# Kernel tuning notes

Hardware: AMD Instinct MI355X
Metric: run time of the kernel (lower is better)

## Reference

```python
import jax, jax.numpy as jnp
from jax import lax
import numpy as np

B, S, G = 16, 384, 384
N = S + G
E_CHAR, D = 100, 128
H = D // 2              # LSTM hidden per direction
NHEAD, NHID = 4, 64
T = 21                  # crf_input_dim = label_alphabet.size() + 1
START, STOP = T - 2, T - 1
ALPHA = 0.2
CHAR_V, GAZ_V = 8000, 100000
NEG = -9e15             # pyGAT masked_fill value


def setup_inputs():
    key = jax.random.key(0)
    ks = jax.random.split(key, 20)
    f32 = jnp.float32
    def nrm(k, shape, s=0.05):
        return (jax.random.normal(k, shape) * s).astype(f32)
    eye = jnp.eye(N, dtype=bool)
    def adj(k):
        return ((jax.random.uniform(k, (B, N, N)) < 0.1) | eye[None]).astype(jnp.int32)
    return dict(
        batch_char=jax.random.randint(ks[0], (B, S), 0, CHAR_V),
        batch_len=jnp.full((B,), S, jnp.int32),
        gaz_list=jax.random.randint(ks[1], (B, G), 0, GAZ_V),
        t_graph=adj(ks[2]), c_graph=adj(ks[3]), l_graph=adj(ks[4]),
        mask=jnp.ones((B, S), jnp.int32),
        char_table=nrm(ks[5], (CHAR_V, E_CHAR)),
        gaz_table=nrm(ks[6], (GAZ_V, D)),
        w_ih_f=nrm(ks[7], (4 * H, E_CHAR)), w_hh_f=nrm(ks[8], (4 * H, H)),
        b_f=jnp.zeros((4 * H,), f32),
        w_ih_b=nrm(ks[9], (4 * H, E_CHAR)), w_hh_b=nrm(ks[10], (4 * H, H)),
        b_b=jnp.zeros((4 * H,), f32),
        h2h_W=nrm(ks[11], (T, D)), h2h_b=jnp.zeros((T,), f32),
        gat_Wh=nrm(ks[12], (3, NHEAD, D, NHID)),
        gat_ah=nrm(ks[13], (3, NHEAD, 2 * NHID)),
        gat_Wo=nrm(ks[14], (3, NHEAD * NHID, T)),
        gat_ao=nrm(ks[15], (3, 2 * T)),
        fuse_w=jnp.ones((4,), f32),
        transitions=nrm(ks[16], (T, T)),
    )


def _lstm_dir(x, w_ih, w_hh, b, reverse):
    # x: [B,S,E]; torch gate order i,f,g,o
    Bb = x.shape[0]
    Hh = w_hh.shape[1]
    xw = jnp.einsum('bse,ge->bsg', x, w_ih) + b
    def step(carry, xt):
        h, c = carry
        g = xt + h @ w_hh.T
        i, f, gg, o = jnp.split(g, 4, axis=-1)
        c = jax.nn.sigmoid(f) * c + jax.nn.sigmoid(i) * jnp.tanh(gg)
        h = jax.nn.sigmoid(o) * jnp.tanh(c)
        return (h, c), h
    h0 = jnp.zeros((Bb, Hh), x.dtype)
    _, hs = lax.scan(step, (h0, h0), xw.swapaxes(0, 1), reverse=reverse)
    return hs.swapaxes(0, 1)


def _gat_layer(x, adj, W, a, concat):
    # pyGAT batched layer: e_ij = LeakyReLU(a . [Wh_i || Wh_j]), masked softmax over j
    h = jnp.einsum('bnd,df->bnf', x, W)
    F_ = W.shape[1]
    f1 = h @ a[:F_]           # [B,N]
    f2 = h @ a[F_:]
    e = jax.nn.leaky_relu(f1[:, :, None] + f2[:, None, :], negative_slope=ALPHA)
    e = jnp.where(adj > 0, e, NEG)
    att = jax.nn.softmax(e, axis=-1)
    out = jnp.einsum('bij,bjf->bif', att, h)
    return jax.nn.elu(out) if concat else out


def _gat(x, adj, Wh, ah, Wo, ao):
    heads = jax.vmap(lambda W, a: _gat_layer(x, adj, W, a, True))(Wh, ah)  # [H,B,N,F]
    hcat = jnp.moveaxis(heads, 0, 2).reshape(x.shape[0], x.shape[1], -1)
    return jax.nn.elu(_gat_layer(hcat, adj, Wo, ao, False))


def _crf_feature(batch_char, gaz_list, graphs, char_table, gaz_table,
                 w_ih_f, w_hh_f, b_f, w_ih_b, w_hh_b, b_b, h2h_W, h2h_b,
                 gat_Wh, gat_ah, gat_Wo, gat_ao, fuse_w):
    emb = char_table[batch_char]                      # [B,S,E_CHAR]
    hf = _lstm_dir(emb, w_ih_f, w_hh_f, b_f, False)
    hb = _lstm_dir(emb, w_ih_b, w_hh_b, b_b, True)
    lstm_feat = jnp.concatenate([hf, hb], axis=-1)    # [B,S,D]
    gaz_feat = gaz_table[gaz_list]                    # [B,G,D]
    gat_in = jnp.concatenate([lstm_feat, gaz_feat], axis=1)  # [B,N,D]
    gat_outs = [_gat(gat_in, adj, gat_Wh[k], gat_ah[k], gat_Wo[k], gat_ao[k])[:, :S]
                for k, adj in enumerate(graphs)]
    lstm_proj = lstm_feat @ h2h_W.T + h2h_b           # [B,S,T]
    return (fuse_w[0] * lstm_proj + fuse_w[1] * gat_outs[0]
            + fuse_w[2] * gat_outs[1] + fuse_w[3] * gat_outs[2])


def _viterbi(feats, transitions, mask):
    Bb, Ss, Tt = feats.shape
    ids = jnp.arange(Tt)
    part0 = feats[:, 0, :] + transitions[START][None, :]
    def step(part, inp):
        feat_t, m_t = inp
        cur = part[:, :, None] + transitions[None] + feat_t[:, None, :]  # [B,prev,cur]
        new = cur.max(axis=1)
        bp = cur.argmax(axis=1)
        m = (m_t > 0)[:, None]
        return jnp.where(m, new, part), jnp.where(m, bp, ids[None, :])
    part, bps = lax.scan(step, part0,
                         (feats[:, 1:].swapaxes(0, 1), mask[:, 1:].swapaxes(0, 1)))
    last_tag = jnp.argmax(part + transitions[:, STOP][None, :], axis=1)
    def back(tag, bp):
        prev = jnp.take_along_axis(bp, tag[:, None], axis=1)[:, 0]
        return prev, prev
    _, prevs = lax.scan(back, last_tag, bps, reverse=True)   # prevs[j] = tag at time j
    return jnp.concatenate([prevs.swapaxes(0, 1), last_tag[:, None]], axis=1)


def reference(batch_char, batch_len, gaz_list, t_graph, c_graph, l_graph, mask,
              char_table, gaz_table, w_ih_f, w_hh_f, b_f, w_ih_b, w_hh_b, b_b,
              h2h_W, h2h_b, gat_Wh, gat_ah, gat_Wo, gat_ao, fuse_w, transitions):
    # batch_len is all == S (mask all ones), so packed BiLSTM == plain BiLSTM
    feats = _crf_feature(batch_char, gaz_list, (t_graph, c_graph, l_graph),
                         char_table, gaz_table, w_ih_f, w_hh_f, b_f,
                         w_ih_b, w_hh_b, b_b, h2h_W, h2h_b,
                         gat_Wh, gat_ah, gat_Wo, gat_ao, fuse_w)
    return _viterbi(feats, transitions, mask)
```

## Files before the change

kernel.cpp:

```cpp
#include <hip/hip_runtime.h>
#include <hip/hip_bf16.h>
#include <cstdint>
#include <cstddef>

#define BB 16
#define SS 384
#define GG 384
#define NN 768
#define DD 128
#define EC 100
#define TT 21
#define NHEADS 4
#define BN (BB*NN)
#define BS (BB*SS)

typedef float v2f __attribute__((ext_vector_type(2)));

__device__ __forceinline__ float sigf(float x) { return 1.0f / (1.0f + __expf(-x)); }
__device__ __forceinline__ float tanh_fast(float x) {
    return 1.0f - 2.0f / (__expf(2.0f * x) + 1.0f);
}
__device__ __forceinline__ float wred_max(float v) {
    #pragma unroll
    for (int o = 32; o > 0; o >>= 1) v = fmaxf(v, __shfl_xor(v, o));
    return v;
}
__device__ __forceinline__ float wred_sum(float v) {
    #pragma unroll
    for (int o = 32; o > 0; o >>= 1) v += __shfl_xor(v, o);
    return v;
}
__device__ __forceinline__ float rlane(float v, int l) {
    return __uint_as_float(__builtin_amdgcn_readlane(__float_as_uint(v), l));
}

__global__ __launch_bounds__(256) void k_xw(
    const int* __restrict__ batch_char, const float* __restrict__ char_table,
    const float* __restrict__ w_ih_f, const float* __restrict__ b_f,
    const float* __restrict__ w_ih_b, const float* __restrict__ b_b,
    float* __restrict__ xw_f, float* __restrict__ xw_b)
{
    __shared__ float At[EC * 68];
    __shared__ float Bt[EC * 68];
    __shared__ int   chs[64];
    const int tid = threadIdx.x;
    const int rt  = blockIdx.x;
    const int ot  = blockIdx.y;
    const int dir = ot >> 2, gt = ot & 3;
    const float* wih  = dir ? w_ih_b : w_ih_f;
    const float* bias = dir ? b_b    : b_f;
    float*       out  = dir ? xw_b   : xw_f;

    if (tid < 64) chs[tid] = batch_char[rt * 64 + tid];
    __syncthreads();
    for (int idx = tid; idx < 64 * EC; idx += 256) {
        int r = idx / EC, e = idx - r * EC;
        At[e * 68 + r] = char_table[(size_t)chs[r] * EC + e];
        Bt[e * 68 + r] = wih[(size_t)(gt * 64 + r) * EC + e];
    }
    __syncthreads();

    const int ty = tid >> 4, tx = tid & 15;
    const int r0 = ty * 4, c0 = tx * 4;
    float acc[4][4] = {};
    #pragma unroll 4
    for (int e = 0; e < EC; ++e) {
        float4 a = *(const float4*)&At[e * 68 + r0];
        float4 bv = *(const float4*)&Bt[e * 68 + c0];
        float av[4] = {a.x, a.y, a.z, a.w};
        float bb[4] = {bv.x, bv.y, bv.z, bv.w};
        #pragma unroll
        for (int i = 0; i < 4; ++i)
            #pragma unroll
            for (int j = 0; j < 4; ++j) acc[i][j] = fmaf(av[i], bb[j], acc[i][j]);
    }
    #pragma unroll
    for (int i = 0; i < 4; ++i) {
        int row = rt * 64 + r0 + i;
        int gc  = gt * 64 + c0;
        float4 o;
        o.x = acc[i][0] + bias[gc + 0];
        o.y = acc[i][1] + bias[gc + 1];
        o.z = acc[i][2] + bias[gc + 2];
        o.w = acc[i][3] + bias[gc + 3];
        *(float4*)&out[(size_t)row * 256 + gc] = o;
    }
}

__global__ __launch_bounds__(256) void k_gaz(
    const int* __restrict__ gaz_list, const float* __restrict__ gaz_table,
    float* __restrict__ gat_in)
{
    int idx = blockIdx.x * 256 + threadIdx.x;
    int d = idx & 127;
    int rest = idx >> 7;
    int g = rest % GG;
    int b = rest / GG;
    float v = gaz_table[(size_t)gaz_list[b * GG + g] * DD + d];
    gat_in[((size_t)b * NN + SS + g) * DD + d] = v;
}

__global__ __launch_bounds__(64, 1) void k_lstm(
    const float* __restrict__ xw_f, const float* __restrict__ xw_b,
    const float* __restrict__ w_hh_f, const float* __restrict__ w_hh_b,
    float* __restrict__ gat_in)
{
    const int lane = threadIdx.x;
    const int b = blockIdx.x >> 1, dir = blockIdx.x & 1;
    const float* xw  = (dir ? xw_b : xw_f) + (size_t)b * SS * 256;
    const float* whh = dir ? w_hh_b : w_hh_f;

    v2f w2[4][32];
    #pragma unroll
    for (int g = 0; g < 4; ++g) {
        const float4* r4 = (const float4*)(whh + (size_t)(g * 64 + lane) * 64);
        #pragma unroll
        for (int q = 0; q < 16; ++q) {
            float4 v = r4[q];
            w2[g][2 * q]     = v2f{v.x, v.y};
            w2[g][2 * q + 1] = v2f{v.z, v.w};
        }
    }

    float h = 0.f, c = 0.f;
    const int t0 = dir ? (SS - 1) : 0;
    float x0 = xw[t0 * 256 +   0 + lane];
    float x1 = xw[t0 * 256 +  64 + lane];
    float x2 = xw[t0 * 256 + 128 + lane];
    float x3 = xw[t0 * 256 + 192 + lane];
    float* outp = gat_in + ((size_t)b * NN) * DD + dir * 64 + lane;

    for (int tt = 0; tt < SS; ++tt) {
        const int t = dir ? (SS - 1 - tt) : tt;
        const int tn = dir ? (t - 1) : (t + 1);
        float nx0 = 0.f, nx1 = 0.f, nx2 = 0.f, nx3 = 0.f;
        if (tt + 1 < SS) {
            nx0 = xw[tn * 256 +   0 + lane];
            nx1 = xw[tn * 256 +  64 + lane];
            nx2 = xw[tn * 256 + 128 + lane];
            nx3 = xw[tn * 256 + 192 + lane];
        }
        v2f a0 = v2f{x0, 0.f}, a1 = v2f{x1, 0.f};
        v2f a2 = v2f{x2, 0.f}, a3 = v2f{x3, 0.f};
        #pragma unroll
        for (int j = 0; j < 32; ++j) {
            v2f hp = v2f{rlane(h, 2 * j), rlane(h, 2 * j + 1)};
            a0 = __builtin_elementwise_fma(hp, w2[0][j], a0);
            a1 = __builtin_elementwise_fma(hp, w2[1][j], a1);
            a2 = __builtin_elementwise_fma(hp, w2[2][j], a2);
            a3 = __builtin_elementwise_fma(hp, w2[3][j], a3);
        }
        float gi = a0.x + a0.y, gf = a1.x + a1.y;
        float gg = a2.x + a2.y, go = a3.x + a3.y;
        float nc = sigf(gf) * c + sigf(gi) * tanh_fast(gg);
        h = sigf(go) * tanh_fast(nc);
        c = nc;
        outp[(size_t)t * DD] = h;
        x0 = nx0; x1 = nx1; x2 = nx2; x3 = nx3;
    }
}

__global__ __launch_bounds__(256) void k_p1(
    const float* __restrict__ gat_in, const float* __restrict__ gat_Wh,
    const float* __restrict__ gat_ah, int k,
    float* __restrict__ h1, float* __restrict__ f1g, float* __restrict__ f2g)
{
    __shared__ float At[64 * 68];
    __shared__ float Bt[64 * 68];
    __shared__ float sf1[64], sf2[64];
    const int tid = threadIdx.x;
    const int rt = blockIdx.x, hd = blockIdx.y;
    if (tid < 64) { sf1[tid] = 0.f; sf2[tid] = 0.f; }
    const float* W = gat_Wh + ((size_t)(k * NHEADS + hd)) * DD * 64;
    const int ty = tid >> 4, tx = tid & 15;
    const int r0 = ty * 4, c0 = tx * 4;
    float acc[4][4] = {};
    for (int ph = 0; ph < 2; ++ph) {
        __syncthreads();
        for (int idx = tid; idx < 64 * 64; idx += 256) {
            int r = idx >> 6, e = idx & 63;
            At[e * 68 + r] = gat_in[((size_t)(rt * 64 + r)) * DD + ph * 64 + e];
            Bt[e * 68 + r] = W[(size_t)(ph * 64 + e) * 64 + r];
        }
        __syncthreads();
        #pragma unroll 4
        for (int e = 0; e < 64; ++e) {
            float4 a = *(const float4*)&At[e * 68 + r0];
            float4 bv = *(const float4*)&Bt[e * 68 + c0];
            float av[4] = {a.x, a.y, a.z, a.w};
            float bb[4] = {bv.x, bv.y, bv.z, bv.w};
            #pragma unroll
            for (int i = 0; i < 4; ++i)
                #pragma unroll
                for (int j = 0; j < 4; ++j) acc[i][j] = fmaf(av[i], bb[j], acc[i][j]);
        }
    }
    const float* ah = gat_ah + (size_t)(k * NHEADS + hd) * 128;
    float a1[4], a2[4];
    #pragma unroll
    for (int j = 0; j < 4; ++j) { a1[j] = ah[c0 + j]; a2[j] = ah[64 + c0 + j]; }
    #pragma unroll
    for (int i = 0; i < 4; ++i) {
        int n = rt * 64 + r0 + i;
        float4 o = make_float4(acc[i][0], acc[i][1], acc[i][2], acc[i][3]);
        *(float4*)&h1[((size_t)n * NHEADS + hd) * 64 + c0] = o;
        float p1 = acc[i][0] * a1[0] + acc[i][1] * a1[1] + acc[i][2] * a1[2] + acc[i][3] * a1[3];
        float p2 = acc[i][0] * a2[0] + acc[i][1] * a2[1] + acc[i][2] * a2[2] + acc[i][3] * a2[3];
        atomicAdd(&sf1[r0 + i], p1);
        atomicAdd(&sf2[r0 + i], p2);
    }
    __syncthreads();
    if (tid < 64) {
        f1g[hd * BN + rt * 64 + tid] = sf1[tid];
        f2g[hd * BN + rt * 64 + tid] = sf2[tid];
    }
}

__global__ __launch_bounds__(256) void k_attn1(
    const int* __restrict__ adj, const float* __restrict__ h1,
    const float* __restrict__ f1g, const float* __restrict__ f2g,
    float* __restrict__ out1, unsigned long long* __restrict__ packed)
{
    __shared__ int   nbr[NN];
    __shared__ float ep[NHEADS][NN];
    __shared__ unsigned long long wm[12];
    __shared__ int cntS;
    const int tid = threadIdx.x, wave = tid >> 6, lane = tid & 63;
    const int n = blockIdx.x;
    const int b = n / NN;
    #pragma unroll
    for (int it = 0; it < 3; ++it) {
        int j = it * 256 + tid;
        int a = adj[(size_t)n * NN + j];
        unsigned long long m = __ballot(a > 0);
        if (lane == 0) { wm[it * 4 + wave] = m; packed[(size_t)n * 12 + it * 4 + wave] = m; }
    }
    __syncthreads();
    if (wave == 0) {
        unsigned long long m = (lane < 12) ? wm[lane] : 0ULL;
        int pc = __popcll(m);
        int inc = pc;
        #pragma unroll
        for (int d = 1; d < 16; d <<= 1) { int t = __shfl_up(inc, d); if (lane >= d) inc += t; }
        int C = __shfl(inc, 11);
        if (lane == 0) cntS = C;
        int off = inc - pc;
        while (m) {
            int bit = __builtin_ctzll(m);
            nbr[off++] = lane * 64 + bit;
            m &= m - 1;
        }
    }
    __syncthreads();
    const int C = cntS;
    const int hd = wave;
    const float f1 = f1g[hd * BN + n];
    const float* f2p = f2g + hd * BN + b * NN;
    float mx = -3.0e38f;
    for (int t = lane; t < C; t += 64) {
        float e = f1 + f2p[nbr[t]];
        e = (e >= 0.f) ? e : 0.2f * e;
        ep[hd][t] = e;
        mx = fmaxf(mx, e);
    }
    mx = wred_max(mx);
    float sum = 0.f;
    for (int t = lane; t < C; t += 64) {
        float p = __expf(ep[hd][t] - mx);
        ep[hd][t] = p;
        sum += p;
    }
    sum = wred_sum(sum);
    const float* hb = h1 + (size_t)b * NN * (NHEADS * 64) + hd * 64 + lane;
    float ac0 = 0.f, ac1 = 0.f, ac2 = 0.f, ac3 = 0.f;
    int t = 0;
    for (; t + 3 < C; t += 4) {
        int j0 = nbr[t], j1 = nbr[t + 1], j2 = nbr[t + 2], j3 = nbr[t + 3];
        float p0 = ep[hd][t], p1 = ep[hd][t + 1], p2 = ep[hd][t + 2], p3 = ep[hd][t + 3];
        ac0 = fmaf(p0, hb[(size_t)j0 * 256], ac0);
        ac1 = fmaf(p1, hb[(size_t)j1 * 256], ac1);
        ac2 = fmaf(p2, hb[(size_t)j2 * 256], ac2);
        ac3 = fmaf(p3, hb[(size_t)j3 * 256], ac3);
    }
    for (; t < C; ++t) ac0 = fmaf(ep[hd][t], hb[(size_t)nbr[t] * 256], ac0);
    float r = ((ac0 + ac1) + (ac2 + ac3)) / sum;
    r = (r > 0.f) ? r : expm1f(r);
    out1[(size_t)n * 256 + hd * 64 + lane] = r;
}

__global__ __launch_bounds__(256) void k_p2(
    const float* __restrict__ out1, const float* __restrict__ gat_Wo,
    const float* __restrict__ gat_ao, int k,
    float* __restrict__ h2, float* __restrict__ f1o, float* __restrict__ f2o)
{
    __shared__ float ld[12 * 256];
    __shared__ float lf1[12], lf2[12];
    const int tid = threadIdx.x;
    const int blk = blockIdx.x;
    if (tid < 12) { lf1[tid] = 0.f; lf2[tid] = 0.f; }
    for (int idx = tid; idx < 12 * 256; idx += 256)
        ld[idx] = out1[(size_t)blk * 12 * 256 + idx];
    __syncthreads();
    if (tid < 252) {
        const int r = tid / TT, c = tid - r * TT;
        const float* Wo = gat_Wo + (size_t)k * 256 * TT;
        const float4* row4 = (const float4*)&ld[r * 256];
        float acc = 0.f;
        #pragma unroll 8
        for (int q4 = 0; q4 < 64; ++q4) {
            float4 v = row4[q4];
            int q = q4 * 4;
            acc = fmaf(v.x, Wo[(q + 0) * TT + c], acc);
            acc = fmaf(v.y, Wo[(q + 1) * TT + c], acc);
            acc = fmaf(v.z, Wo[(q + 2) * TT + c], acc);
            acc = fmaf(v.w, Wo[(q + 3) * TT + c], acc);
        }
        const int n = blk * 12 + r;
        h2[(size_t)n * TT + c] = acc;
        const float* ao = gat_ao + k * 2 * TT;
        atomicAdd(&lf1[r], acc * ao[c]);
        atomicAdd(&lf2[r], acc * ao[TT + c]);
    }
    __syncthreads();
    if (tid < 12) {
        f1o[blk * 12 + tid] = lf1[tid];
        f2o[blk * 12 + tid] = lf2[tid];
    }
}

__global__ __launch_bounds__(64) void k_attn2(
    const unsigned long long* __restrict__ packed,
    const float* __restrict__ h2, const float* __restrict__ f1o,
    const float* __restrict__ f2o, float* __restrict__ out2k)
{
    __shared__ int   nbr[NN];
    __shared__ float ep[NN];
    const int lane = threadIdx.x;
    const int blk = blockIdx.x;
    const int b = blk / SS, s = blk - b * SS;
    const int n = b * NN + s;
    unsigned long long w64 = (lane < 12) ? packed[(size_t)n * 12 + lane] : 0ULL;
    int pc = __popcll(w64);
    int inc = pc;
    #pragma unroll
    for (int d = 1; d < 16; d <<= 1) {
        int t = __shfl_up(inc, d, 16);
        if ((lane & 15) >= d) inc += t;
    }
    const int C = __shfl(inc, 11);
    int off = inc - pc;
    while (w64) {
        int bit = __builtin_ctzll(w64);
        nbr[off++] = lane * 64 + bit;
        w64 &= w64 - 1;
    }
    __syncthreads();
    const float f1 = f1o[n];
    const float* f2p = f2o + b * NN;
    float mx = -3.0e38f;
    for (int t = lane; t < C; t += 64) {
        int j = nbr[t];
        float e = f1 + f2p[j];
        e = (e >= 0.f) ? e : 0.2f * e;
        ep[t] = e;
        mx = fmaxf(mx, e);
    }
    mx = wred_max(mx);
    float sum = 0.f;
    for (int t = lane; t < C; t += 64) {
        float p = __expf(ep[t] - mx);
        ep[t] = p;
        sum += p;
    }
    sum = wred_sum(sum);
    const float* h2b = h2 + (size_t)b * NN * TT + ((lane < TT) ? lane : 0);
    float ac0 = 0.f, ac1 = 0.f, ac2 = 0.f, ac3 = 0.f;
    int t = 0;
    for (; t + 3 < C; t += 4) {
        int j0 = nbr[t], j1 = nbr[t + 1], j2 = nbr[t + 2], j3 = nbr[t + 3];
        float p0 = ep[t], p1 = ep[t + 1], p2 = ep[t + 2], p3 = ep[t + 3];
        ac0 = fmaf(p0, h2b[(size_t)j0 * TT], ac0);
        ac1 = fmaf(p1, h2b[(size_t)j1 * TT], ac1);
        ac2 = fmaf(p2, h2b[(size_t)j2 * TT], ac2);
        ac3 = fmaf(p3, h2b[(size_t)j3 * TT], ac3);
    }
    for (; t < C; ++t) ac0 = fmaf(ep[t], h2b[(size_t)nbr[t] * TT], ac0);
    if (lane < TT) {
        float r = ((ac0 + ac1) + (ac2 + ac3)) / sum;
        r = (r > 0.f) ? r : expm1f(r);
        out2k[(size_t)blk * TT + lane] = r;
    }
}

__global__ __launch_bounds__(64) void k_fuse(
    const float* __restrict__ gat_in, const float* __restrict__ h2h_W,
    const float* __restrict__ h2h_b, const float* __restrict__ fuse_w,
    const float* __restrict__ out2, float* __restrict__ feats)
{
    __shared__ float row[DD];
    const int lane = threadIdx.x;
    const int blk = blockIdx.x;
    const int b = blk / SS, s = blk - b * SS;
    const float* src = gat_in + ((size_t)b * NN + s) * DD;
    row[lane] = src[lane];
    row[lane + 64] = src[lane + 64];
    __syncthreads();
    if (lane < TT) {
        float acc = h2h_b[lane];
        const float4* w4 = (const float4*)&h2h_W[lane * DD];
        const float4* r4 = (const float4*)row;
        #pragma unroll 8
        for (int d4 = 0; d4 < 32; ++d4) {
            float4 w = w4[d4]; float4 v = r4[d4];
            acc = fmaf(w.x, v.x, acc); acc = fmaf(w.y, v.y, acc);
            acc = fmaf(w.z, v.z, acc); acc = fmaf(w.w, v.w, acc);
        }
        size_t o = (size_t)blk * TT + lane;
        feats[o] = fuse_w[0] * acc + fuse_w[1] * out2[o]
                 + fuse_w[2] * out2[(size_t)BS * TT + o]
                 + fuse_w[3] * out2[2 * (size_t)BS * TT + o];
    }
}

__global__ __launch_bounds__(64) void k_vit(
    const float* __restrict__ feats, const float* __restrict__ trans,
    int* __restrict__ out)
{
    __shared__ float part[24];
    __shared__ unsigned char bp[SS - 1][24];
    const int lane = threadIdx.x;
    const int b = blockIdx.x;
    const int pg = lane / TT;
    const int c = lane - pg * TT;
    const bool act = (pg < 3);
    const int p0 = pg * 7;
    float tc[7];
    if (act) {
        #pragma unroll
        for (int u = 0; u < 7; ++u) tc[u] = trans[(p0 + u) * TT + c];
    }
    if (lane < TT) part[lane] = feats[((size_t)b * SS) * TT + lane] + trans[19 * TT + lane];
    if (lane >= TT && lane < 24) part[lane] = -3.0e38f;
    __syncthreads();
    for (int t = 1; t < SS; ++t) {
        float best = -3.0e38f; int bi = 0;
        if (act) {
            #pragma unroll
            for (int u = 0; u < 7; ++u) {
                float v = part[p0 + u] + tc[u];
                if (v > best) { best = v; bi = p0 + u; }
            }
        }
        float bv1 = __shfl(best, lane + 21);
        int   bi1 = __shfl(bi,   lane + 21);
        float bv2 = __shfl(best, lane + 42);
        int   bi2 = __shfl(bi,   lane + 42);
        if (lane < TT) {
            if (bv1 > best) { best = bv1; bi = bi1; }
            if (bv2 > best) { best = bv2; bi = bi2; }
            bp[t - 1][lane] = (unsigned char)bi;
            part[lane] = best + feats[((size_t)b * SS + t) * TT + lane];
        }
        __syncthreads();
    }
    float fv = (lane < TT) ? part[lane] + trans[lane * TT + 20] : -3.0e38f;
    int fi = (lane < TT) ? lane : 0;
    #pragma unroll
    for (int o = 32; o > 0; o >>= 1) {
        float ov = __shfl_xor(fv, o);
        int oi = __shfl_xor(fi, o);
        if (ov > fv || (ov == fv && oi < fi)) { fv = ov; fi = oi; }
    }
    __syncthreads();
    if (lane == 0) {
        int cur = fi;
        out[b * SS + SS - 1] = cur;
        for (int u = SS - 2; u >= 0; --u) {
            cur = bp[u][cur];
            out[b * SS + u] = cur;
        }
    }
}

extern "C" void kernel_launch(void* const* d_in, const int* in_sizes, int n_in,
                              void* d_out, int out_size, void* d_ws, size_t ws_size,
                              hipStream_t stream) {
    (void)in_sizes; (void)n_in; (void)out_size; (void)ws_size;
    const int*   batch_char = (const int*)d_in[0];
    const int*   gaz_list   = (const int*)d_in[2];
    const int*   graphs[3]  = {(const int*)d_in[3], (const int*)d_in[4], (const int*)d_in[5]};
    const float* char_table = (const float*)d_in[7];
    const float* gaz_table  = (const float*)d_in[8];
    const float* w_ih_f = (const float*)d_in[9];
    const float* w_hh_f = (const float*)d_in[10];
    const float* b_f    = (const float*)d_in[11];
    const float* w_ih_b = (const float*)d_in[12];
    const float* w_hh_b = (const float*)d_in[13];
    const float* b_b    = (const float*)d_in[14];
    const float* h2h_W  = (const float*)d_in[15];
    const float* h2h_b  = (const float*)d_in[16];
    const float* gat_Wh = (const float*)d_in[17];
    const float* gat_ah = (const float*)d_in[18];
    const float* gat_Wo = (const float*)d_in[19];
    const float* gat_ao = (const float*)d_in[20];
    const float* fuse_w = (const float*)d_in[21];
    const float* trans  = (const float*)d_in[22];

    float* ws = (float*)d_ws;
    float* gat_in = ws;
    float* xw_f   = gat_in + 1572864;
    float* xw_b   = xw_f   + 1572864;
    float* h1     = xw_b   + 1572864;
    float* out1   = h1     + 3145728;
    float* h2     = out1   + 3145728;
    float* f1g    = h2     + 258048;
    float* f2g    = f1g    + 49152;
    float* f1o    = f2g    + 49152;
    float* f2o    = f1o    + 12288;
    float* out2   = f2o    + 12288;
    float* feats  = out2   + 387072;
    unsigned long long* packed = (unsigned long long*)(feats + 129024);

    k_xw<<<dim3(96, 8), 256, 0, stream>>>(batch_char, char_table, w_ih_f, b_f,
                                          w_ih_b, b_b, xw_f, xw_b);
    k_gaz<<<3072, 256, 0, stream>>>(gaz_list, gaz_table, gat_in);
    k_lstm<<<32, 64, 0, stream>>>(xw_f, xw_b, w_hh_f, w_hh_b, gat_in);
    for (int k = 0; k < 3; ++k) {
        k_p1<<<dim3(192, 4), 256, 0, stream>>>(gat_in, gat_Wh, gat_ah, k, h1, f1g, f2g);
        k_attn1<<<BN, 256, 0, stream>>>(graphs[k], h1, f1g, f2g, out1, packed);
        k_p2<<<1024, 256, 0, stream>>>(out1, gat_Wo, gat_ao, k, h2, f1o, f2o);
        k_attn2<<<BS, 64, 0, stream>>>(packed, h2, f1o, f2o, out2 + (size_t)k * BS * TT);
    }
    k_fuse<<<BS, 64, 0, stream>>>(gat_in, h2h_W, h2h_b, fuse_w, out2, feats);
    k_vit<<<BB, 64, 0, stream>>>(feats, trans, (int*)d_out);
}
```

Before: 1.050 ms.

## Split LSTM recurrence across four waves with LDS hidden-state exchange

The BiLSTM recurrence kernel now runs with 256 threads per block instead of one wave. Each lane holds one weight row (one gate, one hidden unit), so a step needs 32 FMAs per lane instead of 128, and the new hidden state is exchanged through shared memory. The precomputed input projections are staged into shared memory in 32-step chunks with asynchronous global-to-LDS loads. Outputs are written back in batched float4 stores from a ring buffer. In exchange, every timestep now pays a block-wide barrier and LDS round trips, which may offset the shorter FMA chain.

Result: faster. 976.8 us (-7.0%).

```diff
diff --git a/kernel.cpp b/kernel.cpp
--- a/kernel.cpp
+++ b/kernel.cpp
@@ -30,8 +30,10 @@
     for (int o = 32; o > 0; o >>= 1) v += __shfl_xor(v, o);
     return v;
 }
-__device__ __forceinline__ float rlane(float v, int l) {
-    return __uint_as_float(__builtin_amdgcn_readlane(__float_as_uint(v), l));
+__device__ __forceinline__ void gl_lds16(const float* gsrc, float* ldst) {
+    __builtin_amdgcn_global_load_lds(
+        (const __attribute__((address_space(1))) void*)gsrc,
+        (__attribute__((address_space(3))) void*)ldst, 16, 0, 0);
 }
 
 __global__ __launch_bounds__(256) void k_xw(
@@ -100,63 +102,111 @@
     gat_in[((size_t)b * NN + SS + g) * DD + d] = v;
 }
 
-__global__ __launch_bounds__(64, 1) void k_lstm(
+__global__ __launch_bounds__(256, 1) void k_lstm(
     const float* __restrict__ xw_f, const float* __restrict__ xw_b,
     const float* __restrict__ w_hh_f, const float* __restrict__ w_hh_b,
     float* __restrict__ gat_in)
 {
-    const int lane = threadIdx.x;
+    __shared__ __align__(16) float xwc[64][256];
+    __shared__ __align__(16) float hist[64][64];
+    const int tid = threadIdx.x, w = tid >> 6, l = tid & 63;
     const int b = blockIdx.x >> 1, dir = blockIdx.x & 1;
+    const int g = l >> 4, u = w * 16 + (l & 15);
     const float* xw  = (dir ? xw_b : xw_f) + (size_t)b * SS * 256;
     const float* whh = dir ? w_hh_b : w_hh_f;
-
-    v2f w2[4][32];
-    #pragma unroll
-    for (int g = 0; g < 4; ++g) {
-        const float4* r4 = (const float4*)(whh + (size_t)(g * 64 + lane) * 64);
+    float* gout = gat_in + ((size_t)b * NN) * DD + dir * 64;
+
+    v2f wr[32];
+    {
+        const float4* r4 = (const float4*)(whh + (size_t)(g * 64 + u) * 64);
         #pragma unroll
         for (int q = 0; q < 16; ++q) {
             float4 v = r4[q];
-            w2[g][2 * q]     = v2f{v.x, v.y};
-            w2[g][2 * q + 1] = v2f{v.z, v.w};
-        }
-    }
-
-    float h = 0.f, c = 0.f;
-    const int t0 = dir ? (SS - 1) : 0;
-    float x0 = xw[t0 * 256 +   0 + lane];
-    float x1 = xw[t0 * 256 +  64 + lane];
-    float x2 = xw[t0 * 256 + 128 + lane];
-    float x3 = xw[t0 * 256 + 192 + lane];
-    float* outp = gat_in + ((size_t)b * NN) * DD + dir * 64 + lane;
+            wr[2 * q]     = v2f{v.x, v.y};
+            wr[2 * q + 1] = v2f{v.z, v.w};
+        }
+    }
+    if (tid < 64) hist[63][tid] = 0.f;
+
+    {
+        const int gt0 = dir ? (SS - 32) : 0;
+        #pragma unroll
+        for (int r = 0; r < 8; ++r) {
+            int s = w * 8 + r;
+            int lrow = dir ? (31 - s) : s;
+            gl_lds16(xw + (size_t)(gt0 + s) * 256 + l * 4, &xwc[lrow][0]);
+        }
+    }
+    __syncthreads();
+
+    float c = 0.f;
+    const int xoff = g * 64 + u;
 
     for (int tt = 0; tt < SS; ++tt) {
-        const int t = dir ? (SS - 1 - tt) : tt;
-        const int tn = dir ? (t - 1) : (t + 1);
-        float nx0 = 0.f, nx1 = 0.f, nx2 = 0.f, nx3 = 0.f;
-        if (tt + 1 < SS) {
-            nx0 = xw[tn * 256 +   0 + lane];
-            nx1 = xw[tn * 256 +  64 + lane];
-            nx2 = xw[tn * 256 + 128 + lane];
-            nx3 = xw[tn * 256 + 192 + lane];
-        }
-        v2f a0 = v2f{x0, 0.f}, a1 = v2f{x1, 0.f};
-        v2f a2 = v2f{x2, 0.f}, a3 = v2f{x3, 0.f};
-        #pragma unroll
-        for (int j = 0; j < 32; ++j) {
-            v2f hp = v2f{rlane(h, 2 * j), rlane(h, 2 * j + 1)};
-            a0 = __builtin_elementwise_fma(hp, w2[0][j], a0);
-            a1 = __builtin_elementwise_fma(hp, w2[1][j], a1);
-            a2 = __builtin_elementwise_fma(hp, w2[2][j], a2);
-            a3 = __builtin_elementwise_fma(hp, w2[3][j], a3);
-        }
-        float gi = a0.x + a0.y, gf = a1.x + a1.y;
-        float gg = a2.x + a2.y, go = a3.x + a3.y;
+        if ((tt & 31) == 0) {
+            const int ch = tt >> 5;
+            if (ch + 1 < SS / 32) {
+                const int c1 = ch + 1;
+                const int gt0 = dir ? (SS - (c1 + 1) * 32) : (c1 * 32);
+                #pragma unroll
+                for (int r = 0; r < 8; ++r) {
+                    int s = w * 8 + r;
+                    int lrow = ((c1 * 32) + (dir ? (31 - s) : s)) & 63;
+                    gl_lds16(xw + (size_t)(gt0 + s) * 256 + l * 4, &xwc[lrow][0]);
+                }
+            }
+            if (ch >= 1) {
+                const int cf = ch - 1;
+                int i = tid >> 3;
+                int col = (tid & 7) * 8;
+                int row = (cf * 32 + i) & 63;
+                int t = dir ? (SS - 1 - (cf * 32 + i)) : (cf * 32 + i);
+                float4 v0 = *(const float4*)&hist[row][col];
+                float4 v1 = *(const float4*)&hist[row][col + 4];
+                *(float4*)&gout[(size_t)t * DD + col] = v0;
+                *(float4*)&gout[(size_t)t * DD + col + 4] = v1;
+            }
+        }
+        const float4* h4 = (const float4*)hist[(tt - 1) & 63];
+        float x = xwc[tt & 63][xoff];
+        v2f hv[32];
+        #pragma unroll
+        for (int q = 0; q < 16; ++q) {
+            float4 hq = h4[q];
+            hv[2 * q]     = v2f{hq.x, hq.y};
+            hv[2 * q + 1] = v2f{hq.z, hq.w};
+        }
+        v2f s0{0.f, 0.f}, s1{0.f, 0.f}, s2{0.f, 0.f}, s3{0.f, 0.f};
+        #pragma unroll
+        for (int j = 0; j < 8; ++j) {
+            s0 = __builtin_elementwise_fma(hv[j],      wr[j],      s0);
+            s1 = __builtin_elementwise_fma(hv[j + 8],  wr[j + 8],  s1);
+            s2 = __builtin_elementwise_fma(hv[j + 16], wr[j + 16], s2);
+            s3 = __builtin_elementwise_fma(hv[j + 24], wr[j + 24], s3);
+        }
+        v2f sv = (s0 + s1) + (s2 + s3);
+        float gv = sv.x + sv.y + x;
+        const int srcl = l & 15;
+        float gi = __shfl(gv, srcl);
+        float gf = __shfl(gv, srcl + 16);
+        float gg = __shfl(gv, srcl + 32);
+        float go = __shfl(gv, srcl + 48);
         float nc = sigf(gf) * c + sigf(gi) * tanh_fast(gg);
-        h = sigf(go) * tanh_fast(nc);
+        float nh = sigf(go) * tanh_fast(nc);
         c = nc;
-        outp[(size_t)t * DD] = h;
-        x0 = nx0; x1 = nx1; x2 = nx2; x3 = nx3;
+        if (l < 16) hist[tt & 63][u] = nh;
+        __syncthreads();
+    }
+    {
+        const int cf = SS / 32 - 1;
+        int i = tid >> 3;
+        int col = (tid & 7) * 8;
+        int row = (cf * 32 + i) & 63;
+        int t = dir ? (SS - 1 - (cf * 32 + i)) : (cf * 32 + i);
+        float4 v0 = *(const float4*)&hist[row][col];
+        float4 v1 = *(const float4*)&hist[row][col + 4];
+        *(float4*)&gout[(size_t)t * DD + col] = v0;
+        *(float4*)&gout[(size_t)t * DD + col + 4] = v1;
     }
 }
 
@@ -524,7 +574,7 @@
     k_xw<<<dim3(96, 8), 256, 0, stream>>>(batch_char, char_table, w_ih_f, b_f,
                                           w_ih_b, b_b, xw_f, xw_b);
     k_gaz<<<3072, 256, 0, stream>>>(gaz_list, gaz_table, gat_in);
-    k_lstm<<<32, 64, 0, stream>>>(xw_f, xw_b, w_hh_f, w_hh_b, gat_in);
+    k_lstm<<<32, 256, 0, stream>>>(xw_f, xw_b, w_hh_f, w_hh_b, gat_in);
     for (int k = 0; k < 3; ++k) {
         k_p1<<<dim3(192, 4), 256, 0, stream>>>(gat_in, gat_Wh, gat_ah, k, h1, f1g, f2g);
         k_attn1<<<BN, 256, 0, stream>>>(graphs[k], h1, f1g, f2g, out1, packed);
```
